# Kernel tuning notes

Measured on AMD Instinct MI355X. Metric: run time of the kernel, lower is better.

Reference implementation:

```python
import jax, jax.numpy as jnp
import numpy as np


def setup_inputs() -> dict:
    key = jax.random.key(0)
    ks = jax.random.split(key, 8)
    C = 256
    C8 = C // 8
    B, H, W = 8, 64, 64
    scale = 0.05
    return {
        "x": jax.random.normal(ks[0], (B, C, W, H), dtype=jnp.float32),
        "Wq": jax.random.normal(ks[1], (C8, C), dtype=jnp.float32) * scale,
        "bq": jax.random.normal(ks[2], (C8,), dtype=jnp.float32) * scale,
        "Wk": jax.random.normal(ks[3], (C8, C), dtype=jnp.float32) * scale,
        "bk": jax.random.normal(ks[4], (C8,), dtype=jnp.float32) * scale,
        "Wv": jax.random.normal(ks[5], (C, C), dtype=jnp.float32) * scale,
        "bv": jax.random.normal(ks[6], (C,), dtype=jnp.float32) * scale,
        "gamma": jax.random.normal(ks[7], (1,), dtype=jnp.float32),
    }


def reference(x, Wq, bq, Wk, bk, Wv, bv, gamma):
    B, C, W, H = x.shape
    N = W * H
    xf = x.reshape(B, C, N)  # flatten spatial dims: [B, C, N]
    # 1x1 convs == per-pixel channel matmuls
    q = jnp.einsum("oc,bcn->bno", Wq, xf) + bq  # [B, N, C/8]
    k = jnp.einsum("oc,bcn->bon", Wk, xf) + bk[None, :, None]  # [B, C/8, N]
    v = jnp.einsum("oc,bcn->bon", Wv, xf) + bv[None, :, None]  # [B, C, N]
    # unscaled QK^T softmax (dim=-1), as in the original
    attn = jax.nn.softmax(jnp.einsum("bno,bom->bnm", q, k), axis=-1)  # [B, N, N]
    # out[b,c,m] = sum_n v[b,c,n] * attn[b,m,n]
    out = jnp.einsum("bcn,bmn->bcm", v, attn).reshape(B, C, W, H)
    return gamma[0] * out + x
```

## Files before the change

kernel.cpp:

```cpp
#include <hip/hip_runtime.h>
#include <stdint.h>

#define B_ 8
#define C_ 256
#define N_ 4096

typedef __attribute__((ext_vector_type(8))) short short8;
typedef __attribute__((ext_vector_type(4))) float float4v;
typedef __attribute__((ext_vector_type(16))) float floatx16;

__device__ __forceinline__ uint16_t f2bfr(float f) {
  return (uint16_t)((__float_as_uint(f) + 0x8000u) >> 16);
}
__device__ __forceinline__ uint32_t pkbf(float lo, float hi) {
  return ((__float_as_uint(hi) + 0x8000u) & 0xffff0000u) |
         ((__float_as_uint(lo) + 0x8000u) >> 16);
}
__device__ __forceinline__ float ex2(float x) {
  return __builtin_amdgcn_exp2f(x);
}
__device__ __forceinline__ short8 ld8(const uint16_t* p) {
  union { ushort4 h[2]; short8 v; } u;
  u.h[0] = *reinterpret_cast<const ushort4*>(p);
  u.h[1] = *reinterpret_cast<const ushort4*>(p + 4);
  return u.v;
}

__global__ __launch_bounds__(256) void wconv_kernel(
    const float* __restrict__ Wq, const float* __restrict__ bq,
    const float* __restrict__ Wk, const float* __restrict__ bk,
    const float* __restrict__ Wv, const float* __restrict__ bv,
    uint16_t* __restrict__ Wc, float* __restrict__ bc)
{
  const float L2E = 1.44269504088896f;
  int tg = blockIdx.x * 256 + threadIdx.x;
  int idx = tg * 4;
  const float* src = (idx < 8192) ? (Wq + idx)
                   : (idx < 16384) ? (Wk + (idx - 8192))
                                   : (Wv + (idx - 16384));
  float sc = (idx < 8192) ? L2E : 1.0f;
  float4 wv = *reinterpret_cast<const float4*>(src);
  uint2 o;
  o.x = pkbf(wv.x * sc, wv.y * sc);
  o.y = pkbf(wv.z * sc, wv.w * sc);
  *reinterpret_cast<uint2*>(Wc + idx) = o;
  if (tg < 320)
    bc[tg] = (tg < 32) ? bq[tg] * L2E : (tg < 64) ? bk[tg - 32] : bv[tg - 64];
}

__global__ __launch_bounds__(512, 4) void qkv_mfma(
    const float* __restrict__ x, const uint16_t* __restrict__ Wc,
    const float* __restrict__ bc,
    uint16_t* __restrict__ Qw, uint16_t* __restrict__ Kw, uint16_t* __restrict__ Vw)
{
  __shared__ __align__(16) uint16_t xs[64][268];
  const int b = blockIdx.x & 7;
  const int tile = blockIdx.x >> 3;
  const int n0 = tile * 64;
  const int tid = threadIdx.x;
  const int nl = tid & 63, grp = tid >> 6;
  const int w = grp, l15 = tid & 15, q = (tid & 63) >> 4;
  const int nb = w & 3;

  const float* xb = x + (size_t)b * C_ * N_ + n0;
  #pragma unroll
  for (int it = 0; it < 16; ++it) {
    int c2 = it * 16 + grp * 2;
    float f0 = xb[(size_t)c2 * N_ + nl];
    float f1 = xb[(size_t)(c2 + 1) * N_ + nl];
    *reinterpret_cast<uint32_t*>(&xs[nl][c2]) = pkbf(f0, f1);
  }
  __syncthreads();

  float4v acc[10];
  #pragma unroll
  for (int i = 0; i < 10; ++i) acc[i] = (float4v){0.f, 0.f, 0.f, 0.f};

  const int ob0 = (w >> 2) * 10;
  #pragma unroll
  for (int h2 = 0; h2 < 2; ++h2) {
    short8 bx[4];
    #pragma unroll
    for (int kb = 0; kb < 4; ++kb)
      bx[kb] = ld8(&xs[nb * 16 + l15][h2 * 128 + kb * 32 + q * 8]);
    #pragma unroll
    for (int oi = 0; oi < 10; ++oi) {
      int ob = ob0 + oi;
      const uint16_t* wr = Wc + (size_t)(ob * 16 + l15) * 256 + h2 * 128 + q * 8;
      short8 aw[4];
      #pragma unroll
      for (int kb = 0; kb < 4; ++kb)
        aw[kb] = *reinterpret_cast<const short8*>(wr + kb * 32);
      #pragma unroll
      for (int kb = 0; kb < 4; ++kb)
        acc[oi] = __builtin_amdgcn_mfma_f32_16x16x32_bf16(aw[kb], bx[kb], acc[oi], 0, 0, 0);
    }
  }

  __syncthreads();
  uint16_t (*qs)[72] = reinterpret_cast<uint16_t(*)[72]>(&xs[0][0]);
  if (w < 4) {
    #pragma unroll
    for (int oi = 0; oi < 4; ++oi) {
      float4v a = acc[oi];
      const float* bb = bc + oi * 16 + q * 4;
      uint2 pk2;
      pk2.x = pkbf(a.x + bb[0], a.y + bb[1]);
      pk2.y = pkbf(a.z + bb[2], a.w + bb[3]);
      *reinterpret_cast<uint2*>(&qs[nb * 16 + l15][oi * 16 + q * 4]) = pk2;
    }
  }
  __syncthreads();
  if (tid < 256) {
    int n = tid >> 2, sub = tid & 3;
    const uint16_t* row = qs[n];
    uint4 d0 = *reinterpret_cast<const uint4*>(&row[sub * 16]);
    uint4 d1 = *reinterpret_cast<const uint4*>(&row[sub * 16 + 8]);
    size_t nn = (size_t)b * N_ + n0 + n;
    if (sub < 2) {
      uint4* dst = reinterpret_cast<uint4*>(Qw + nn * 32 + sub * 16);
      dst[0] = d0; dst[1] = d1;
    } else {
      uint4* dst = reinterpret_cast<uint4*>(Kw + nn * 32 + (sub - 2) * 16);
      dst[0] = d0; dst[1] = d1;
    }
  }
  const size_t blk = ((size_t)b * 64 + tile) * 4;
  const int half = l15 >> 3;
  const int podd = l15 & 1, s2 = (l15 >> 1) & 1;
  const int nq = (l15 & 7) & ~3;
  #pragma unroll
  for (int oi = 0; oi < 10; ++oi) {
    int ob = ob0 + oi;
    if (ob < 4) continue;
    float4v a = acc[oi];
    const float* bb = bc + ob * 16 + q * 4;
    int cb = ob * 16 - 64 + q * 4;
    float v0 = a.x + bb[0], v1 = a.y + bb[1];
    float v2 = a.z + bb[2], v3 = a.w + bb[3];
    float t0 = __shfl_xor(v0, 1), t1 = __shfl_xor(v1, 1);
    float t2 = __shfl_xor(v2, 1), t3 = __shfl_xor(v3, 1);
    uint32_t wA = podd ? pkbf(t2, v2) : pkbf(v0, t0);
    uint32_t wB = podd ? pkbf(t3, v3) : pkbf(v1, t1);
    uint32_t uA = __shfl_xor(wA, 2), uB = __shfl_xor(wB, 2);
    uint2 st;
    int cfin;
    if (!s2) { st.x = wA; st.y = uA; cfin = cb + 2 * podd; }
    else     { st.x = uB; st.y = wB; cfin = cb + 2 * podd + 1; }
    size_t vaddr = (blk + (cfin >> 6)) * 4096
                 + (size_t)(nb * 1024 + ((cfin >> 5) & 1) * 512 + half * 256
                            + (cfin & 31) * 8 + nq);
    *reinterpret_cast<uint2*>(Vw + vaddr) = st;
  }
}

__global__ __launch_bounds__(512, 4) void attn_mfma(
    const uint16_t* __restrict__ Qw, const uint16_t* __restrict__ Kw,
    const uint16_t* __restrict__ Vw, const float* __restrict__ x,
    const float* __restrict__ gamma, float* __restrict__ out)
{
  __shared__ __align__(16) union Smem {
    uint16_t Ps[2][64 * 76];
    float Os[128 * 69];
  } sm;
  __shared__ float Ls[64];

  const int b = blockIdx.x & 7;
  const int m0 = (blockIdx.x >> 3) * 64;
  const int tid = threadIdx.x;
  const int w = tid >> 6, lane = tid & 63;
  const int l15 = lane & 15, q = lane >> 4;
  const int l31 = lane & 31, half = lane >> 5;
  const int nb = w & 3, mbp = (w >> 2) * 2;

  const uint16_t* Kb = Kw + (size_t)b * N_ * 32 + (size_t)(nb * 16 + l15) * 32 + q * 8;
  const short8 qf0 = *reinterpret_cast<const short8*>(
      Qw + ((size_t)b * N_ + m0 + (mbp    ) * 16 + l15) * 32 + q * 8);
  const short8 qf1 = *reinterpret_cast<const short8*>(
      Qw + ((size_t)b * N_ + m0 + (mbp + 1) * 16 + l15) * 32 + q * 8);
  const uint16_t* Vb = Vw + ((size_t)b * 256 + (w >> 1)) * 4096
                     + (w & 1) * 512 + half * 256 + l31 * 8;

  floatx16 O[2];
  #pragma unroll
  for (int i = 0; i < 16; ++i) { O[0][i] = 0.f; O[1][i] = 0.f; }
  float rs0 = 0.f, rs1 = 0.f;
  const float4v zero4 = (float4v){0.f, 0.f, 0.f, 0.f};
  if (tid < 64) Ls[tid] = 0.f;

  short8 vc[4];
  #pragma unroll
  for (int ks = 0; ks < 4; ++ks)
    vc[ks] = *reinterpret_cast<const short8*>(Vb + ks * 1024);
  short8 kc = *reinterpret_cast<const short8*>(Kb + (size_t)64 * 32);
  {
    short8 kf = *reinterpret_cast<const short8*>(Kb);
    float4v s0 = __builtin_amdgcn_mfma_f32_16x16x32_bf16(kf, qf0, zero4, 0, 0, 0);
    float4v s1 = __builtin_amdgcn_mfma_f32_16x16x32_bf16(kf, qf1, zero4, 0, 0, 0);
    float p0 = ex2(s0.x), p1 = ex2(s0.y), p2 = ex2(s0.z), p3 = ex2(s0.w);
    rs0 += (p0 + p1) + (p2 + p3);
    uint2 pw; pw.x = pkbf(p0, p1); pw.y = pkbf(p2, p3);
    *reinterpret_cast<uint2*>(&sm.Ps[0][((mbp)*16 + l15) * 76 + nb * 16 + q * 4]) = pw;
    float r0 = ex2(s1.x), r1 = ex2(s1.y), r2 = ex2(s1.z), r3 = ex2(s1.w);
    rs1 += (r0 + r1) + (r2 + r3);
    uint2 rw; rw.x = pkbf(r0, r1); rw.y = pkbf(r2, r3);
    *reinterpret_cast<uint2*>(&sm.Ps[0][((mbp + 1)*16 + l15) * 76 + nb * 16 + q * 4]) = rw;
  }
  __syncthreads();

  for (int t = 0; t < 64; ++t) {
    const int buf = t & 1;

    short8 vn[4];
    if (t < 63) {
      const uint16_t* vt = Vb + (size_t)(t + 1) * 16384;
      #pragma unroll
      for (int ks = 0; ks < 4; ++ks)
        vn[ks] = *reinterpret_cast<const short8*>(vt + ks * 1024);
    }
    short8 kn;
    if (t < 62)
      kn = *reinterpret_cast<const short8*>(Kb + (size_t)(t + 2) * 64 * 32);

    if (t < 63) {
      float4v s0 = __builtin_amdgcn_mfma_f32_16x16x32_bf16(kc, qf0, zero4, 0, 0, 0);
      float4v s1 = __builtin_amdgcn_mfma_f32_16x16x32_bf16(kc, qf1, zero4, 0, 0, 0);
      float p0 = ex2(s0.x), p1 = ex2(s0.y), p2 = ex2(s0.z), p3 = ex2(s0.w);
      rs0 += (p0 + p1) + (p2 + p3);
      uint2 pw; pw.x = pkbf(p0, p1); pw.y = pkbf(p2, p3);
      *reinterpret_cast<uint2*>(&sm.Ps[buf ^ 1][((mbp)*16 + l15) * 76 + nb * 16 + q * 4]) = pw;
      float r0 = ex2(s1.x), r1 = ex2(s1.y), r2 = ex2(s1.z), r3 = ex2(s1.w);
      rs1 += (r0 + r1) + (r2 + r3);
      uint2 rw; rw.x = pkbf(r0, r1); rw.y = pkbf(r2, r3);
      *reinterpret_cast<uint2*>(&sm.Ps[buf ^ 1][((mbp + 1)*16 + l15) * 76 + nb * 16 + q * 4]) = rw;
    }

    #pragma unroll
    for (int ks = 0; ks < 4; ++ks) {
      short8 pa0 = ld8(&sm.Ps[buf][(l31     ) * 76 + ks * 16 + half * 8]);
      short8 pa1 = ld8(&sm.Ps[buf][(32 + l31) * 76 + ks * 16 + half * 8]);
      O[0] = __builtin_amdgcn_mfma_f32_32x32x16_bf16(pa0, vc[ks], O[0], 0, 0, 0);
      O[1] = __builtin_amdgcn_mfma_f32_32x32x16_bf16(pa1, vc[ks], O[1], 0, 0, 0);
    }
    __syncthreads();

    if (t < 63) {
      #pragma unroll
      for (int ks = 0; ks < 4; ++ks) vc[ks] = vn[ks];
    }
    if (t < 62) kc = kn;
  }

  rs0 += __shfl_xor(rs0, 16); rs0 += __shfl_xor(rs0, 32);
  rs1 += __shfl_xor(rs1, 16); rs1 += __shfl_xor(rs1, 32);
  if (q == 0) {
    atomicAdd(&Ls[(mbp    ) * 16 + l15], rs0);
    atomicAdd(&Ls[(mbp + 1) * 16 + l15], rs1);
  }
  __syncthreads();
  if (tid < 64) Ls[tid] = gamma[0] / Ls[tid];
  __syncthreads();

  #pragma unroll
  for (int chunk = 0; chunk < 2; ++chunk) {
    if ((w >> 2) == chunk) {
      int cl = (w & 3) * 32 + l31;
      #pragma unroll
      for (int h = 0; h < 2; ++h)
        #pragma unroll
        for (int reg = 0; reg < 16; ++reg) {
          int m = h * 32 + (reg & 3) + 8 * (reg >> 2) + 4 * half;
          sm.Os[cl * 69 + m] = O[h][reg] * Ls[m];
        }
    }
    __syncthreads();
    {
      int cl = tid >> 2, msub = tid & 3;
      int c = chunk * 128 + cl;
      size_t idx = ((size_t)b * C_ + c) * N_ + m0 + msub * 16;
      const float* os = &sm.Os[cl * 69 + msub * 16];
      #pragma unroll
      for (int i = 0; i < 4; ++i) {
        float4 xv = *reinterpret_cast<const float4*>(x + idx + i * 4);
        float4 ov;
        ov.x = os[i * 4 + 0] + xv.x;
        ov.y = os[i * 4 + 1] + xv.y;
        ov.z = os[i * 4 + 2] + xv.z;
        ov.w = os[i * 4 + 3] + xv.w;
        *reinterpret_cast<float4*>(out + idx + i * 4) = ov;
      }
    }
    __syncthreads();
  }
}

extern "C" void kernel_launch(void* const* d_in, const int* in_sizes, int n_in,
                              void* d_out, int out_size, void* d_ws, size_t ws_size,
                              hipStream_t stream) {
  const float* x     = (const float*)d_in[0];
  const float* Wq    = (const float*)d_in[1];
  const float* bq    = (const float*)d_in[2];
  const float* Wk    = (const float*)d_in[3];
  const float* bk    = (const float*)d_in[4];
  const float* Wv    = (const float*)d_in[5];
  const float* bv    = (const float*)d_in[6];
  const float* gamma = (const float*)d_in[7];
  float* out = (float*)d_out;

  uint16_t* Qw = (uint16_t*)d_ws;
  uint16_t* Kw = Qw + (size_t)B_ * N_ * 32;
  uint16_t* Vw = Kw + (size_t)B_ * N_ * 32;
  uint16_t* Wc = Vw + (size_t)B_ * C_ * N_;
  float*    bc = (float*)(Wc + 320 * 256);

  wconv_kernel<<<80, 256, 0, stream>>>(Wq, bq, Wk, bk, Wv, bv, Wc, bc);
  qkv_mfma<<<512, 512, 0, stream>>>(x, Wc, bc, Qw, Kw, Vw);
  attn_mfma<<<512, 512, 0, stream>>>(Qw, Kw, Vw, x, gamma, out);
}
```

Measured before the change: 225.2 us.

## Use 32x32 MFMA tiles in QKV projection and stage V through LDS

The QKV projection kernel switches from 16x16x32 MFMA tiles (ten output blocks per wave) to 32x32x16 tiles. Each wave now owns 32 V channels across all 64 pixels, and four waves also compute Q/K. The V output is written to shared memory first and then stored to global memory with 16-byte coalesced writes, replacing the shuffle-based 8-byte scattered stores. The goal is fewer redundant weight loads and better store coalescing, at the cost of extra LDS traffic, another barrier, and unbalanced work between waves.

```diff
diff --git a/kernel.cpp b/kernel.cpp
--- a/kernel.cpp
+++ b/kernel.cpp
@@ -53,14 +53,21 @@
     const float* __restrict__ bc,
     uint16_t* __restrict__ Qw, uint16_t* __restrict__ Kw, uint16_t* __restrict__ Vw)
 {
-  __shared__ __align__(16) uint16_t xs[64][268];
+  __shared__ __align__(16) union Smem {
+    uint16_t xs[64][268];
+    struct {
+      uint16_t qs[64][72];
+      uint16_t vs[256][68];
+    } e;
+  } sm;
+
   const int b = blockIdx.x & 7;
   const int tile = blockIdx.x >> 3;
   const int n0 = tile * 64;
   const int tid = threadIdx.x;
   const int nl = tid & 63, grp = tid >> 6;
-  const int w = grp, l15 = tid & 15, q = (tid & 63) >> 4;
-  const int nb = w & 3;
+  const int w = grp, lane = tid & 63;
+  const int l31 = lane & 31, half = lane >> 5;
 
   const float* xb = x + (size_t)b * C_ * N_ + n0;
   #pragma unroll
@@ -68,52 +75,56 @@
     int c2 = it * 16 + grp * 2;
     float f0 = xb[(size_t)c2 * N_ + nl];
     float f1 = xb[(size_t)(c2 + 1) * N_ + nl];
-    *reinterpret_cast<uint32_t*>(&xs[nl][c2]) = pkbf(f0, f1);
-  }
-  __syncthreads();
-
-  float4v acc[10];
-  #pragma unroll
-  for (int i = 0; i < 10; ++i) acc[i] = (float4v){0.f, 0.f, 0.f, 0.f};
-
-  const int ob0 = (w >> 2) * 10;
-  #pragma unroll
-  for (int h2 = 0; h2 < 2; ++h2) {
-    short8 bx[4];
-    #pragma unroll
-    for (int kb = 0; kb < 4; ++kb)
-      bx[kb] = ld8(&xs[nb * 16 + l15][h2 * 128 + kb * 32 + q * 8]);
-    #pragma unroll
-    for (int oi = 0; oi < 10; ++oi) {
-      int ob = ob0 + oi;
-      const uint16_t* wr = Wc + (size_t)(ob * 16 + l15) * 256 + h2 * 128 + q * 8;
-      short8 aw[4];
-      #pragma unroll
-      for (int kb = 0; kb < 4; ++kb)
-        aw[kb] = *reinterpret_cast<const short8*>(wr + kb * 32);
-      #pragma unroll
-      for (int kb = 0; kb < 4; ++kb)
-        acc[oi] = __builtin_amdgcn_mfma_f32_16x16x32_bf16(aw[kb], bx[kb], acc[oi], 0, 0, 0);
-    }
-  }
-
-  __syncthreads();
-  uint16_t (*qs)[72] = reinterpret_cast<uint16_t(*)[72]>(&xs[0][0]);
+    *reinterpret_cast<uint32_t*>(&sm.xs[nl][c2]) = pkbf(f0, f1);
+  }
+  __syncthreads();
+
+  floatx16 accV0, accV1, accQ;
+  #pragma unroll
+  for (int i = 0; i < 16; ++i) { accV0[i] = 0.f; accV1[i] = 0.f; accQ[i] = 0.f; }
+
+  const uint16_t* wrV = Wc + (size_t)(64 + w * 32 + l31) * 256 + half * 8;
+  const int qct = w >> 1, qnt = w & 1;
+  const uint16_t* wrQ = Wc + (size_t)(qct * 32 + l31) * 256 + half * 8;
+
+  #pragma unroll
+  for (int kk = 0; kk < 16; ++kk) {
+    short8 aV = *reinterpret_cast<const short8*>(wrV + kk * 16);
+    short8 b0 = ld8(&sm.xs[l31     ][kk * 16 + half * 8]);
+    short8 b1 = ld8(&sm.xs[32 + l31][kk * 16 + half * 8]);
+    accV0 = __builtin_amdgcn_mfma_f32_32x32x16_bf16(aV, b0, accV0, 0, 0, 0);
+    accV1 = __builtin_amdgcn_mfma_f32_32x32x16_bf16(aV, b1, accV1, 0, 0, 0);
+    if (w < 4) {
+      short8 aQ = *reinterpret_cast<const short8*>(wrQ + kk * 16);
+      accQ = __builtin_amdgcn_mfma_f32_32x32x16_bf16(aQ, qnt ? b1 : b0, accQ, 0, 0, 0);
+    }
+  }
+  __syncthreads();
+
   if (w < 4) {
     #pragma unroll
-    for (int oi = 0; oi < 4; ++oi) {
-      float4v a = acc[oi];
-      const float* bb = bc + oi * 16 + q * 4;
+    for (int q4 = 0; q4 < 4; ++q4) {
+      int cb = qct * 32 + q4 * 8 + half * 4;
+      const float* bb = bc + cb;
       uint2 pk2;
-      pk2.x = pkbf(a.x + bb[0], a.y + bb[1]);
-      pk2.y = pkbf(a.z + bb[2], a.w + bb[3]);
-      *reinterpret_cast<uint2*>(&qs[nb * 16 + l15][oi * 16 + q * 4]) = pk2;
-    }
-  }
-  __syncthreads();
+      pk2.x = pkbf(accQ[q4 * 4 + 0] + bb[0], accQ[q4 * 4 + 1] + bb[1]);
+      pk2.y = pkbf(accQ[q4 * 4 + 2] + bb[2], accQ[q4 * 4 + 3] + bb[3]);
+      *reinterpret_cast<uint2*>(&sm.e.qs[qnt * 32 + l31][cb]) = pk2;
+    }
+  }
+  #pragma unroll
+  for (int reg = 0; reg < 16; ++reg) {
+    int cl = (reg & 3) + 8 * (reg >> 2) + 4 * half;
+    int cp = w * 32 + cl;
+    float bias = bc[64 + cp];
+    sm.e.vs[cp][l31     ] = f2bfr(accV0[reg] + bias);
+    sm.e.vs[cp][32 + l31] = f2bfr(accV1[reg] + bias);
+  }
+  __syncthreads();
+
   if (tid < 256) {
     int n = tid >> 2, sub = tid & 3;
-    const uint16_t* row = qs[n];
+    const uint16_t* row = sm.e.qs[n];
     uint4 d0 = *reinterpret_cast<const uint4*>(&row[sub * 16]);
     uint4 d1 = *reinterpret_cast<const uint4*>(&row[sub * 16 + 8]);
     size_t nn = (size_t)b * N_ + n0 + n;
@@ -126,31 +137,16 @@
     }
   }
   const size_t blk = ((size_t)b * 64 + tile) * 4;
-  const int half = l15 >> 3;
-  const int podd = l15 & 1, s2 = (l15 >> 1) & 1;
-  const int nq = (l15 & 7) & ~3;
-  #pragma unroll
-  for (int oi = 0; oi < 10; ++oi) {
-    int ob = ob0 + oi;
-    if (ob < 4) continue;
-    float4v a = acc[oi];
-    const float* bb = bc + ob * 16 + q * 4;
-    int cb = ob * 16 - 64 + q * 4;
-    float v0 = a.x + bb[0], v1 = a.y + bb[1];
-    float v2 = a.z + bb[2], v3 = a.w + bb[3];
-    float t0 = __shfl_xor(v0, 1), t1 = __shfl_xor(v1, 1);
-    float t2 = __shfl_xor(v2, 1), t3 = __shfl_xor(v3, 1);
-    uint32_t wA = podd ? pkbf(t2, v2) : pkbf(v0, t0);
-    uint32_t wB = podd ? pkbf(t3, v3) : pkbf(v1, t1);
-    uint32_t uA = __shfl_xor(wA, 2), uB = __shfl_xor(wB, 2);
-    uint2 st;
-    int cfin;
-    if (!s2) { st.x = wA; st.y = uA; cfin = cb + 2 * podd; }
-    else     { st.x = uB; st.y = wB; cfin = cb + 2 * podd + 1; }
-    size_t vaddr = (blk + (cfin >> 6)) * 4096
-                 + (size_t)(nb * 1024 + ((cfin >> 5) & 1) * 512 + half * 256
-                            + (cfin & 31) * 8 + nq);
-    *reinterpret_cast<uint2*>(Vw + vaddr) = st;
+  #pragma unroll
+  for (int i = 0; i < 4; ++i) {
+    int s = i * 512 + tid;
+    int cp = s & 255, rem = s >> 8;
+    int ks = rem >> 1, h2 = rem & 1;
+    uint4 d = *reinterpret_cast<const uint4*>(&sm.e.vs[cp][ks * 16 + h2 * 8]);
+    size_t vaddr = (blk + (cp >> 6)) * 4096
+                 + (size_t)(ks * 1024 + ((cp >> 5) & 1) * 512 + h2 * 256
+                            + (cp & 31) * 8);
+    *reinterpret_cast<uint4*>(Vw + vaddr) = d;
   }
 }
 
```

Result: faster. 202.6 us (-10.0%).
